# Optimization experiments

Measured on AMD Instinct MI355X. Metric: run time of the kernel, lower is better.

The kernel has to match this reference:

```python
import jax, jax.numpy as jnp
import numpy as np

B, N, F_IN, F_OUT = 64, 1024, 200, 200
NEG_SLOPE = 0.2  # PyG GATConv default


def setup_inputs() -> dict:
    key = jax.random.key(0)
    k1, k2, k3, k4, k5 = jax.random.split(key, 5)
    return {
        "x": jax.random.normal(k1, (B, 1, N, F_IN), dtype=jnp.float32),
        "W": jax.random.normal(k2, (F_IN, F_OUT), dtype=jnp.float32) * 0.05,
        "att_src": jax.random.normal(k3, (F_OUT,), dtype=jnp.float32) * 0.05,
        "att_dst": jax.random.normal(k4, (F_OUT,), dtype=jnp.float32) * 0.05,
        "bias": jax.random.normal(k5, (F_OUT,), dtype=jnp.float32) * 0.05,
    }


def reference(x, W, att_src, att_dst, bias):
    # x: [B, 1, N, F_IN]; module flattens to (B*N) nodes but the edge_index
    # only spans node ids 0..N-1 (complete graph minus self loops). PyG's
    # GATConv re-adds self loops for ALL B*N nodes, so:
    #   nodes 0..N-1 : dense softmax attention over all N nodes (incl. self)
    #   nodes >= N   : only the self loop -> out = h_i + bias
    b, _, n, f = x.shape
    xf = x.reshape(b * n, f)
    h = xf @ W                                # [B*N, F_OUT] linear transform

    h0 = h[:n]                                # first graph's nodes
    a_s = h0 @ att_src                        # [N] per-source score
    a_d = h0 @ att_dst                        # [N] per-target score
    # score[i, j] = leaky_relu(a_dst[i] + a_src[j]), softmax over sources j
    scores = jax.nn.leaky_relu(a_d[:, None] + a_s[None, :], negative_slope=NEG_SLOPE)
    alpha = jax.nn.softmax(scores, axis=1)    # [N, N]
    out0 = alpha @ h0 + bias                  # [N, F_OUT]

    out_rest = h[n:] + bias                   # self-loop only -> alpha == 1
    out = jnp.concatenate([out0, out_rest], axis=0)
    return out.reshape(b, n, -1)[:, None]     # [B, 1, N, F_OUT]
```

## Files before the change

### kernel.cpp

```cpp
#include <hip/hip_runtime.h>

#define BATCH 64
#define NNODE 1024
#define FDIM  200
#define MROWS (BATCH * NNODE)
#define NEG_SLOPE 0.2f

#define NKT 7
#define NNT 13

typedef short s16x8 __attribute__((ext_vector_type(8)));
typedef float f32x4 __attribute__((ext_vector_type(4)));


__device__ __forceinline__ unsigned int f2bf(float f) {
    unsigned int u = __float_as_uint(f);
    return (u + 0x7fffu + ((u >> 16) & 1u)) >> 16;
}
__device__ __forceinline__ unsigned int pack2(float a, float b) {
    return f2bf(a) | (f2bf(b) << 16);
}

__global__ __launch_bounds__(64) void k_prep(const float* __restrict__ W,
                                             unsigned short* __restrict__ fragW,
                                             float* __restrict__ a_s,
                                             float* __restrict__ a_d)
{
    const int b    = blockIdx.x;
    const int kt   = b / NNT;
    const int nt   = b - kt * NNT;
    const int lane = threadIdx.x;
    const int n    = nt * 16 + (lane & 15);
    const int kb   = kt * 32 + (lane >> 4) * 8;

    s16x8 v;
    #pragma unroll
    for (int j = 0; j < 8; ++j) {
        int k = kb + j;
        float f = (k < FDIM && n < FDIM) ? W[k * FDIM + n] : 0.f;
        v[j] = (short)f2bf(f);
    }
    ((s16x8*)(fragW + (size_t)b * 512))[lane] = v;

    if (b == 0) {
        for (int i = lane; i < NNODE; i += 64) { a_s[i] = 0.f; a_d[i] = 0.f; }
    }
}

__global__ __launch_bounds__(64) void k_gemm(const float* __restrict__ x,
                                             const unsigned short* __restrict__ fragW,
                                             const float* __restrict__ bias,
                                             const float* __restrict__ att_src,
                                             const float* __restrict__ att_dst,
                                             float* __restrict__ out,
                                             unsigned short* __restrict__ h0frag,
                                             float* __restrict__ a_s,
                                             float* __restrict__ a_d)
{
    __shared__ float scr[16][17];
    const int lane = threadIdx.x;
    const int ln   = lane & 15;
    const int quad = lane >> 4;
    const int R0   = blockIdx.x * 16;

    f32x4 acc[NNT];
    #pragma unroll
    for (int nt = 0; nt < NNT; ++nt) acc[nt] = (f32x4){0.f, 0.f, 0.f, 0.f};

    const float* xrow = x + (size_t)(R0 + ln) * FDIM;

    #pragma unroll
    for (int kt = 0; kt < NKT; ++kt) {
        s16x8 a;
        if (kt < 6 || quad == 0) {
            const float4* ap = (const float4*)(xrow + kt * 32 + quad * 8);
            float4 f0 = ap[0], f1 = ap[1];
            unsigned int d0 = pack2(f0.x, f0.y), d1 = pack2(f0.z, f0.w);
            unsigned int d2 = pack2(f1.x, f1.y), d3 = pack2(f1.z, f1.w);
            unsigned int au[4] = {d0, d1, d2, d3};
            a = *(s16x8*)au;
        } else {
            a = (s16x8){0, 0, 0, 0, 0, 0, 0, 0};
        }
        #pragma unroll
        for (int nt = 0; nt < NNT; ++nt) {
            s16x8 b = *(const s16x8*)(fragW + ((size_t)(kt * NNT + nt) * 64 + lane) * 8);
            acc[nt] = __builtin_amdgcn_mfma_f32_16x16x32_bf16(a, b, acc[nt], 0, 0, 0);
        }
    }

    if (R0 >= NNODE) {
        #pragma unroll
        for (int nt = 0; nt < NNT; ++nt) {
            int col = nt * 16 + ln;
            if (nt < 12 || ln < 8) {
                float bv = bias[col];
                #pragma unroll
                for (int r = 0; r < 4; ++r)
                    out[(size_t)(R0 + quad * 4 + r) * FDIM + col] = acc[nt][r] + bv;
            }
        }
    } else {
        const int kt2 = R0 >> 5;
        const int lo  = (R0 >> 4) & 1;
        for (int nt = 0; nt < NNT; ++nt) {
            #pragma unroll
            for (int r = 0; r < 4; ++r) scr[quad * 4 + r][ln] = acc[nt][r];
            __syncthreads();
            if (lane < 32) {
                int oct = lane >> 4, nl = lane & 15;
                uint4 dv;
                dv.x = pack2(scr[oct * 8 + 0][nl], scr[oct * 8 + 1][nl]);
                dv.y = pack2(scr[oct * 8 + 2][nl], scr[oct * 8 + 3][nl]);
                dv.z = pack2(scr[oct * 8 + 4][nl], scr[oct * 8 + 5][nl]);
                dv.w = pack2(scr[oct * 8 + 6][nl], scr[oct * 8 + 7][nl]);
                *(uint4*)(h0frag + ((size_t)(kt2 * NNT + nt) * 64 + lo * 32 + lane) * 8) = dv;
            }
            __syncthreads();
        }
        float asv[NNT], adv[NNT];
        #pragma unroll
        for (int nt = 0; nt < NNT; ++nt) {
            int col = nt * 16 + ln;
            bool v = (nt < 12 || ln < 8);
            asv[nt] = v ? att_src[col] : 0.f;
            adv[nt] = v ? att_dst[col] : 0.f;
        }
        #pragma unroll
        for (int r = 0; r < 4; ++r) {
            float ps = 0.f, pd = 0.f;
            #pragma unroll
            for (int nt = 0; nt < NNT; ++nt) {
                ps = fmaf(acc[nt][r], asv[nt], ps);
                pd = fmaf(acc[nt][r], adv[nt], pd);
            }
            #pragma unroll
            for (int off = 1; off < 16; off <<= 1) {
                ps += __shfl_xor(ps, off);
                pd += __shfl_xor(pd, off);
            }
            if (ln == 0) {
                atomicAdd(a_s + R0 + quad * 4 + r, ps);
                atomicAdd(a_d + R0 + quad * 4 + r, pd);
            }
        }
        const float4* b4 = (const float4*)bias;
        #pragma unroll
        for (int i = 0; i < 13; ++i) {
            int f = lane + i * 64;
            if (f < 800) {
                int row = f / 50, c4 = f - row * 50;
                ((float4*)out)[(size_t)(R0 + row) * 50 + c4] = b4[c4];
            }
        }
    }
}

__global__ __launch_bounds__(256) void k_stats(const float* __restrict__ a_s,
                                               const float* __restrict__ a_d,
                                               float* __restrict__ m_out,
                                               float* __restrict__ l_out)
{
    __shared__ float as_s[1024];
    const int tid = threadIdx.x;
    #pragma unroll
    for (int i = 0; i < 4; ++i) as_s[tid + i * 256] = a_s[tid + i * 256];
    __syncthreads();

    const int lane = tid & 63;
    const int wv   = tid >> 6;
    const int row  = blockIdx.x * 4 + wv;

    float mx = -1e30f;
    #pragma unroll
    for (int i = 0; i < 16; ++i) mx = fmaxf(mx, as_s[lane + i * 64]);
    #pragma unroll
    for (int off = 32; off; off >>= 1) mx = fmaxf(mx, __shfl_down(mx, off));
    mx = __shfl(mx, 0);

    const float ad = a_d[row];
    float mi = ad + mx; mi = (mi > 0.f) ? mi : NEG_SLOPE * mi;

    float sum = 0.f;
    #pragma unroll
    for (int i = 0; i < 16; ++i) {
        float s = ad + as_s[lane + i * 64];
        s = (s > 0.f) ? s : NEG_SLOPE * s;
        sum += __expf(s - mi);
    }
    #pragma unroll
    for (int off = 32; off; off >>= 1) sum += __shfl_down(sum, off);
    if (lane == 0) { m_out[row] = mi; l_out[row] = sum; }
}

__global__ __launch_bounds__(256) void k_attn(const unsigned short* __restrict__ h0frag,
                                              const float* __restrict__ a_s,
                                              const float* __restrict__ a_d,
                                              const float* __restrict__ m_v,
                                              const float* __restrict__ l_v,
                                              float* __restrict__ out)
{
    const int tid  = threadIdx.x;
    const int lane = tid & 63;
    const int w    = __builtin_amdgcn_readfirstlane(tid >> 6);
    const int ln   = lane & 15;
    const int quad = lane >> 4;
    const int it   = blockIdx.x >> 4;
    const int ks   = blockIdx.x & 15;
    const int i0   = it * 64 + w * 16;
    const int jb   = ks * 64;

    const float ad = a_d[i0 + ln];
    const float mi = m_v[i0 + ln];

    f32x4 acc[NNT];
    #pragma unroll
    for (int nt = 0; nt < NNT; ++nt) acc[nt] = (f32x4){0.f, 0.f, 0.f, 0.f};

    #pragma unroll
    for (int h = 0; h < 2; ++h) {
        const int kt2g = ks * 2 + h;
        const float4* ap = (const float4*)(a_s + jb + h * 32 + quad * 8);
        float4 f0 = ap[0], f1 = ap[1];
        float e[8] = {f0.x, f0.y, f0.z, f0.w, f1.x, f1.y, f1.z, f1.w};
        #pragma unroll
        for (int j = 0; j < 8; ++j) {
            float s = ad + e[j];
            s = (s > 0.f) ? s : NEG_SLOPE * s;
            e[j] = __expf(s - mi);
        }
        unsigned int au[4] = {pack2(e[0], e[1]), pack2(e[2], e[3]),
                              pack2(e[4], e[5]), pack2(e[6], e[7])};
        s16x8 afrag = *(s16x8*)au;
        #pragma unroll
        for (int nt = 0; nt < NNT; ++nt) {
            s16x8 b = *(const s16x8*)(h0frag + ((size_t)(kt2g * NNT + nt) * 64 + lane) * 8);
            acc[nt] = __builtin_amdgcn_mfma_f32_16x16x32_bf16(afrag, b, acc[nt], 0, 0, 0);
        }
    }

    float rl[4];
    #pragma unroll
    for (int r = 0; r < 4; ++r) rl[r] = 1.0f / l_v[i0 + quad * 4 + r];

    #pragma unroll
    for (int nt = 0; nt < NNT; ++nt) {
        int col = nt * 16 + ln;
        if (nt < 12 || ln < 8) {
            #pragma unroll
            for (int r = 0; r < 4; ++r)
                atomicAdd(out + (size_t)(i0 + quad * 4 + r) * FDIM + col,
                          acc[nt][r] * rl[r]);
        }
    }
}

extern "C" void kernel_launch(void* const* d_in, const int* in_sizes, int n_in,
                              void* d_out, int out_size, void* d_ws, size_t ws_size,
                              hipStream_t stream)
{
    const float* x       = (const float*)d_in[0];
    const float* W       = (const float*)d_in[1];
    const float* att_src = (const float*)d_in[2];
    const float* att_dst = (const float*)d_in[3];
    const float* bias    = (const float*)d_in[4];
    float* out = (float*)d_out;
    char*  wsb = (char*)d_ws;

    unsigned short* h0frag = (unsigned short*)(wsb + 0);
    float* a_s   = (float*)(wsb + 425984);
    float* a_d   = (float*)(wsb + 430080);
    float* m_i   = (float*)(wsb + 434176);
    float* l_i   = (float*)(wsb + 438272);
    unsigned short* fragW = (unsigned short*)(wsb + 442368);

    k_prep <<<NKT * NNT,  64, 0, stream>>>(W, fragW, a_s, a_d);
    k_gemm <<<MROWS / 16, 64, 0, stream>>>(x, fragW, bias, att_src, att_dst,
                                           out, h0frag, a_s, a_d);
    k_stats<<<NNODE / 4, 256, 0, stream>>>(a_s, a_d, m_i, l_i);
    k_attn <<<256,       256, 0, stream>>>(h0frag, a_s, a_d, m_i, l_i, out);
}
```

Baseline: 154.5 us.

## Precompute W·att vectors, drop atomics in attention, prefetch GEMM operands

Attention score vectors are now computed as x·(W·att) by a new small kernel, using per-feature vectors produced in the prep kernel, instead of atomically reducing from the GEMM accumulators. The attention kernel is re-split by output column tile over the full source dimension, so it writes output directly with bias and needs no atomics or bias pre-fill. The main GEMM gets register double-buffering of W fragments and early x loads to hide load latency. This adds a kernel launch and redundant reads of the first graph's x, and the attention grid shrinks to fewer blocks with a long serial MFMA chain.

```diff
diff --git a/kernel.cpp b/kernel.cpp
--- a/kernel.cpp
+++ b/kernel.cpp
@@ -22,40 +22,79 @@
 }
 
 __global__ __launch_bounds__(64) void k_prep(const float* __restrict__ W,
+                                             const float* __restrict__ att_src,
+                                             const float* __restrict__ att_dst,
                                              unsigned short* __restrict__ fragW,
-                                             float* __restrict__ a_s,
-                                             float* __restrict__ a_d)
+                                             float* __restrict__ wsv,
+                                             float* __restrict__ wdv)
 {
     const int b    = blockIdx.x;
-    const int kt   = b / NNT;
-    const int nt   = b - kt * NNT;
     const int lane = threadIdx.x;
-    const int n    = nt * 16 + (lane & 15);
-    const int kb   = kt * 32 + (lane >> 4) * 8;
-
-    s16x8 v;
-    #pragma unroll
-    for (int j = 0; j < 8; ++j) {
-        int k = kb + j;
-        float f = (k < FDIM && n < FDIM) ? W[k * FDIM + n] : 0.f;
-        v[j] = (short)f2bf(f);
-    }
-    ((s16x8*)(fragW + (size_t)b * 512))[lane] = v;
-
-    if (b == 0) {
-        for (int i = lane; i < NNODE; i += 64) { a_s[i] = 0.f; a_d[i] = 0.f; }
-    }
+
+    if (b < 91) {
+        const int kt   = b / NNT;
+        const int nt   = b - kt * NNT;
+        const int n    = nt * 16 + (lane & 15);
+        const int kb   = kt * 32 + (lane >> 4) * 8;
+        s16x8 v;
+        #pragma unroll
+        for (int j = 0; j < 8; ++j) {
+            int k = kb + j;
+            float f = (k < FDIM && n < FDIM) ? W[k * FDIM + n] : 0.f;
+            v[j] = (short)f2bf(f);
+        }
+        ((s16x8*)(fragW + (size_t)b * 512))[lane] = v;
+    } else {
+        const int kk = b - 91;
+        const float* Wr = W + kk * FDIM;
+        float ps = 0.f, pd = 0.f;
+        #pragma unroll
+        for (int i = 0; i < 4; ++i) {
+            int n = lane + i * 64;
+            if (n < FDIM) {
+                float wv = Wr[n];
+                ps = fmaf(wv, att_src[n], ps);
+                pd = fmaf(wv, att_dst[n], pd);
+            }
+        }
+        #pragma unroll
+        for (int off = 32; off; off >>= 1) {
+            ps += __shfl_down(ps, off);
+            pd += __shfl_down(pd, off);
+        }
+        if (lane == 0) { wsv[kk] = ps; wdv[kk] = pd; }
+    }
+}
+
+__global__ __launch_bounds__(256) void k_av(const float* __restrict__ x,
+                                            const float* __restrict__ wsv,
+                                            const float* __restrict__ wdv,
+                                            float* __restrict__ a_s,
+                                            float* __restrict__ a_d)
+{
+    const int tid  = threadIdx.x;
+    const int lane = tid & 63;
+    const int row  = blockIdx.x * 4 + (tid >> 6);
+    const float* xr = x + (size_t)row * FDIM;
+    float ss = 0.f, sd = 0.f;
+    for (int k = lane; k < FDIM; k += 64) {
+        float xv = xr[k];
+        ss = fmaf(xv, wsv[k], ss);
+        sd = fmaf(xv, wdv[k], sd);
+    }
+    #pragma unroll
+    for (int off = 32; off; off >>= 1) {
+        ss += __shfl_down(ss, off);
+        sd += __shfl_down(sd, off);
+    }
+    if (lane == 0) { a_s[row] = ss; a_d[row] = sd; }
 }
 
 __global__ __launch_bounds__(64) void k_gemm(const float* __restrict__ x,
                                              const unsigned short* __restrict__ fragW,
                                              const float* __restrict__ bias,
-                                             const float* __restrict__ att_src,
-                                             const float* __restrict__ att_dst,
                                              float* __restrict__ out,
-                                             unsigned short* __restrict__ h0frag,
-                                             float* __restrict__ a_s,
-                                             float* __restrict__ a_d)
+                                             unsigned short* __restrict__ h0frag)
 {
     __shared__ float scr[16][17];
     const int lane = threadIdx.x;
@@ -69,23 +108,51 @@
 
     const float* xrow = x + (size_t)(R0 + ln) * FDIM;
 
+    float4 ar[NKT][2];
+    #pragma unroll
+    for (int kt = 0; kt < 4; ++kt) {
+        const float4* ap = (const float4*)(xrow + kt * 32 + quad * 8);
+        ar[kt][0] = ap[0]; ar[kt][1] = ap[1];
+    }
+
+    s16x8 bc[NNT], bn[NNT];
+    #pragma unroll
+    for (int nt = 0; nt < NNT; ++nt)
+        bc[nt] = *(const s16x8*)(fragW + ((size_t)nt * 64 + lane) * 8);
+
     #pragma unroll
     for (int kt = 0; kt < NKT; ++kt) {
-        s16x8 a;
-        if (kt < 6 || quad == 0) {
-            const float4* ap = (const float4*)(xrow + kt * 32 + quad * 8);
-            float4 f0 = ap[0], f1 = ap[1];
-            unsigned int d0 = pack2(f0.x, f0.y), d1 = pack2(f0.z, f0.w);
-            unsigned int d2 = pack2(f1.x, f1.y), d3 = pack2(f1.z, f1.w);
-            unsigned int au[4] = {d0, d1, d2, d3};
-            a = *(s16x8*)au;
-        } else {
-            a = (s16x8){0, 0, 0, 0, 0, 0, 0, 0};
-        }
-        #pragma unroll
-        for (int nt = 0; nt < NNT; ++nt) {
-            s16x8 b = *(const s16x8*)(fragW + ((size_t)(kt * NNT + nt) * 64 + lane) * 8);
-            acc[nt] = __builtin_amdgcn_mfma_f32_16x16x32_bf16(a, b, acc[nt], 0, 0, 0);
+        if (kt < NKT - 1) {
+            #pragma unroll
+            for (int nt = 0; nt < NNT; ++nt)
+                bn[nt] = *(const s16x8*)(fragW +
+                    ((size_t)((kt + 1) * NNT + nt) * 64 + lane) * 8);
+        }
+        if (kt + 4 < NKT) {
+            int ka = kt + 4;
+            if (ka < 6) {
+                const float4* ap = (const float4*)(xrow + ka * 32 + quad * 8);
+                ar[ka][0] = ap[0]; ar[ka][1] = ap[1];
+            } else {
+                if (quad == 0) {
+                    const float4* ap = (const float4*)(xrow + ka * 32);
+                    ar[ka][0] = ap[0]; ar[ka][1] = ap[1];
+                } else {
+                    ar[ka][0] = make_float4(0.f, 0.f, 0.f, 0.f);
+                    ar[ka][1] = make_float4(0.f, 0.f, 0.f, 0.f);
+                }
+            }
+        }
+        float4 f0 = ar[kt][0], f1 = ar[kt][1];
+        unsigned int au[4] = {pack2(f0.x, f0.y), pack2(f0.z, f0.w),
+                              pack2(f1.x, f1.y), pack2(f1.z, f1.w)};
+        s16x8 a = *(s16x8*)au;
+        #pragma unroll
+        for (int nt = 0; nt < NNT; ++nt)
+            acc[nt] = __builtin_amdgcn_mfma_f32_16x16x32_bf16(a, bc[nt], acc[nt], 0, 0, 0);
+        if (kt < NKT - 1) {
+            #pragma unroll
+            for (int nt = 0; nt < NNT; ++nt) bc[nt] = bn[nt];
         }
     }
 
@@ -118,41 +185,6 @@
             }
             __syncthreads();
         }
-        float asv[NNT], adv[NNT];
-        #pragma unroll
-        for (int nt = 0; nt < NNT; ++nt) {
-            int col = nt * 16 + ln;
-            bool v = (nt < 12 || ln < 8);
-            asv[nt] = v ? att_src[col] : 0.f;
-            adv[nt] = v ? att_dst[col] : 0.f;
-        }
-        #pragma unroll
-        for (int r = 0; r < 4; ++r) {
-            float ps = 0.f, pd = 0.f;
-            #pragma unroll
-            for (int nt = 0; nt < NNT; ++nt) {
-                ps = fmaf(acc[nt][r], asv[nt], ps);
-                pd = fmaf(acc[nt][r], adv[nt], pd);
-            }
-            #pragma unroll
-            for (int off = 1; off < 16; off <<= 1) {
-                ps += __shfl_xor(ps, off);
-                pd += __shfl_xor(pd, off);
-            }
-            if (ln == 0) {
-                atomicAdd(a_s + R0 + quad * 4 + r, ps);
-                atomicAdd(a_d + R0 + quad * 4 + r, pd);
-            }
-        }
-        const float4* b4 = (const float4*)bias;
-        #pragma unroll
-        for (int i = 0; i < 13; ++i) {
-            int f = lane + i * 64;
-            if (f < 800) {
-                int row = f / 50, c4 = f - row * 50;
-                ((float4*)out)[(size_t)(R0 + row) * 50 + c4] = b4[c4];
-            }
-        }
     }
 }
 
@@ -168,8 +200,7 @@
     __syncthreads();
 
     const int lane = tid & 63;
-    const int wv   = tid >> 6;
-    const int row  = blockIdx.x * 4 + wv;
+    const int row  = blockIdx.x * 4 + (tid >> 6);
 
     float mx = -1e30f;
     #pragma unroll
@@ -198,6 +229,7 @@
                                               const float* __restrict__ a_d,
                                               const float* __restrict__ m_v,
                                               const float* __restrict__ l_v,
+                                              const float* __restrict__ bias,
                                               float* __restrict__ out)
 {
     const int tid  = threadIdx.x;
@@ -205,22 +237,19 @@
     const int w    = __builtin_amdgcn_readfirstlane(tid >> 6);
     const int ln   = lane & 15;
     const int quad = lane >> 4;
-    const int it   = blockIdx.x >> 4;
-    const int ks   = blockIdx.x & 15;
+    const int it   = blockIdx.x / NNT;
+    const int nt   = blockIdx.x - it * NNT;
     const int i0   = it * 64 + w * 16;
-    const int jb   = ks * 64;
 
     const float ad = a_d[i0 + ln];
     const float mi = m_v[i0 + ln];
 
-    f32x4 acc[NNT];
-    #pragma unroll
-    for (int nt = 0; nt < NNT; ++nt) acc[nt] = (f32x4){0.f, 0.f, 0.f, 0.f};
-
-    #pragma unroll
-    for (int h = 0; h < 2; ++h) {
-        const int kt2g = ks * 2 + h;
-        const float4* ap = (const float4*)(a_s + jb + h * 32 + quad * 8);
+    f32x4 accA = (f32x4){0.f, 0.f, 0.f, 0.f};
+    f32x4 accB = (f32x4){0.f, 0.f, 0.f, 0.f};
+
+    #pragma unroll
+    for (int kt2 = 0; kt2 < 32; ++kt2) {
+        const float4* ap = (const float4*)(a_s + kt2 * 32 + quad * 8);
         float4 f0 = ap[0], f1 = ap[1];
         float e[8] = {f0.x, f0.y, f0.z, f0.w, f1.x, f1.y, f1.z, f1.w};
         #pragma unroll
@@ -232,25 +261,19 @@
         unsigned int au[4] = {pack2(e[0], e[1]), pack2(e[2], e[3]),
                               pack2(e[4], e[5]), pack2(e[6], e[7])};
         s16x8 afrag = *(s16x8*)au;
-        #pragma unroll
-        for (int nt = 0; nt < NNT; ++nt) {
-            s16x8 b = *(const s16x8*)(h0frag + ((size_t)(kt2g * NNT + nt) * 64 + lane) * 8);
-            acc[nt] = __builtin_amdgcn_mfma_f32_16x16x32_bf16(afrag, b, acc[nt], 0, 0, 0);
-        }
-    }
-
-    float rl[4];
-    #pragma unroll
-    for (int r = 0; r < 4; ++r) rl[r] = 1.0f / l_v[i0 + quad * 4 + r];
-
-    #pragma unroll
-    for (int nt = 0; nt < NNT; ++nt) {
-        int col = nt * 16 + ln;
-        if (nt < 12 || ln < 8) {
-            #pragma unroll
-            for (int r = 0; r < 4; ++r)
-                atomicAdd(out + (size_t)(i0 + quad * 4 + r) * FDIM + col,
-                          acc[nt][r] * rl[r]);
+        s16x8 b = *(const s16x8*)(h0frag + ((size_t)(kt2 * NNT + nt) * 64 + lane) * 8);
+        if (kt2 & 1) accB = __builtin_amdgcn_mfma_f32_16x16x32_bf16(afrag, b, accB, 0, 0, 0);
+        else         accA = __builtin_amdgcn_mfma_f32_16x16x32_bf16(afrag, b, accA, 0, 0, 0);
+    }
+
+    const int col = nt * 16 + ln;
+    if (nt < 12 || ln < 8) {
+        float bv = bias[col];
+        #pragma unroll
+        for (int r = 0; r < 4; ++r) {
+            float rl = 1.0f / l_v[i0 + quad * 4 + r];
+            out[(size_t)(i0 + quad * 4 + r) * FDIM + col]
+                = (accA[r] + accB[r]) * rl + bv;
         }
     }
 }
@@ -273,10 +296,12 @@
     float* m_i   = (float*)(wsb + 434176);
     float* l_i   = (float*)(wsb + 438272);
     unsigned short* fragW = (unsigned short*)(wsb + 442368);
-
-    k_prep <<<NKT * NNT,  64, 0, stream>>>(W, fragW, a_s, a_d);
-    k_gemm <<<MROWS / 16, 64, 0, stream>>>(x, fragW, bias, att_src, att_dst,
-                                           out, h0frag, a_s, a_d);
+    float* wsv   = (float*)(wsb + 535552);
+    float* wdv   = (float*)(wsb + 536352);
+
+    k_prep <<<291,        64, 0, stream>>>(W, att_src, att_dst, fragW, wsv, wdv);
+    k_av   <<<NNODE / 4, 256, 0, stream>>>(x, wsv, wdv, a_s, a_d);
     k_stats<<<NNODE / 4, 256, 0, stream>>>(a_s, a_d, m_i, l_i);
-    k_attn <<<256,       256, 0, stream>>>(h0frag, a_s, a_d, m_i, l_i, out);
-}
+    k_gemm <<<MROWS / 16, 64, 0, stream>>>(x, fragW, bias, out, h0frag);
+    k_attn <<<16 * NNT,  256, 0, stream>>>(h0frag, a_s, a_d, m_i, l_i, bias, out);
+}
```

After: 140.7 us. 9.0% less time.
